# Kernel optimization log

Hardware: AMD Instinct MI355X
Metric: run time of the kernel (lower is better)

The kernel has to match this reference:

```python
import jax, jax.numpy as jnp
import numpy as np

B, T, D, H = 4, 1024, 1024, 16
DH = D // H  # 64

def setup_inputs() -> dict:
    key = jax.random.key(0)
    ks = jax.random.split(key, 5)
    s = 1.0 / np.sqrt(D)
    return {
        "x": jax.random.normal(ks[0], (B, T, D), dtype=jnp.float32),
        "Wqkv": jax.random.uniform(ks[1], (D, 3 * D), dtype=jnp.float32, minval=-s, maxval=s),
        "bqkv": jax.random.uniform(ks[2], (3 * D,), dtype=jnp.float32, minval=-s, maxval=s),
        "Wproj": jax.random.uniform(ks[3], (D, D), dtype=jnp.float32, minval=-s, maxval=s),
        "bproj": jax.random.uniform(ks[4], (D,), dtype=jnp.float32, minval=-s, maxval=s),
        "mask": jnp.ones((B, T), dtype=jnp.int32),
    }

def reference(x, Wqkv, bqkv, Wproj, bproj, mask):
    Bx, Tx, C = x.shape
    qkv = x @ Wqkv + bqkv                      # [B,T,3D]
    q, k, v = jnp.split(qkv, 3, axis=-1)
    # [B,H,T,DH]
    q = q.reshape(Bx, Tx, H, DH).transpose(0, 2, 1, 3)
    k = k.reshape(Bx, Tx, H, DH).transpose(0, 2, 1, 3)
    v = v.reshape(Bx, Tx, H, DH).transpose(0, 2, 1, 3)
    att = jnp.einsum("bhqd,bhkd->bhqk", q, k) / np.sqrt(DH)
    causal = jnp.tril(jnp.ones((Tx, Tx), dtype=bool))          # [T,T]
    keep = causal[None, None] & (mask[:, None, None, :] != 0)  # [B,1,T,T] broadcast
    att = jnp.where(keep, att, -jnp.inf)
    att = jax.nn.softmax(att, axis=-1)
    # dropout is identity in eval / p=0
    out = jnp.einsum("bhqk,bhkd->bhqd", att, v)                # [B,H,T,DH]
    out = out.transpose(0, 2, 1, 3).reshape(Bx, Tx, C)
    return out @ Wproj + bproj
```

## Files before the change

kernel.cpp:

```cpp
#include <hip/hip_runtime.h>
#include <hip/hip_bf16.h>
#include <cstddef>
#include <cstdint>

#define Bb 4
#define Tt 1024
#define Dd 1024
#define Hh 16

typedef __bf16 bf16x8 __attribute__((ext_vector_type(8)));
typedef __bf16 bf16x4 __attribute__((ext_vector_type(4)));
typedef float  f32x4  __attribute__((ext_vector_type(4)));

__device__ __forceinline__ void gload16(const void* g, void* l) {
    __builtin_amdgcn_global_load_lds(
        (const __attribute__((address_space(1))) void*)g,
        (__attribute__((address_space(3))) void*)l, 16, 0, 0);
}

__global__ __launch_bounds__(256) void prep(const float* __restrict__ x,
                                            const float* __restrict__ Wqkv,
                                            const float* __restrict__ Wproj,
                                            __bf16* __restrict__ xb,
                                            __bf16* __restrict__ wqT,
                                            __bf16* __restrict__ wpT) {
    const int bid = blockIdx.x;
    if (bid < 4096) {
        int i = bid * 256 + threadIdx.x;
        float4 v = ((const float4*)x)[i];
        bf16x4 o = { (__bf16)v.x, (__bf16)v.y, (__bf16)v.z, (__bf16)v.w };
        ((bf16x4*)xb)[i] = o;
        return;
    }
    __shared__ float ld[64][65];
    const float* in;
    __bf16* out;
    int K, N, k0, n0;
    if (bid < 4096 + 768) {
        int j = bid - 4096;
        in = Wqkv; out = wqT; K = 1024; N = 3072;
        k0 = (j & 15) * 64; n0 = (j >> 4) * 64;
    } else {
        int j = bid - 4096 - 768;
        in = Wproj; out = wpT; K = 1024; N = 1024;
        k0 = (j & 15) * 64; n0 = (j >> 4) * 64;
    }
    #pragma unroll
    for (int i = 0; i < 16; i++) {
        int idx = i * 256 + threadIdx.x;
        int r = idx >> 6, c = idx & 63;
        ld[r][c] = in[(size_t)(k0 + r) * N + n0 + c];
    }
    __syncthreads();
    #pragma unroll
    for (int i = 0; i < 16; i++) {
        int idx = i * 256 + threadIdx.x;
        int r = idx >> 6, c = idx & 63;
        out[(size_t)(n0 + r) * K + k0 + c] = (__bf16)ld[c][r];
    }
}

__global__ __launch_bounds__(256) void v_transpose(const __bf16* __restrict__ qkv,
                                                   __bf16* __restrict__ vt) {
    __shared__ __bf16 ld[64][65];
    const int t0 = blockIdx.x * 64;
    const int h  = blockIdx.y;
    const int b  = blockIdx.z;
    const size_t src = ((size_t)(b * Tt + t0)) * 3072 + 2048 + h * 64;
    #pragma unroll
    for (int i = 0; i < 16; i++) {
        int idx = i * 256 + threadIdx.x;
        int tr = idx >> 6, dc = idx & 63;
        ld[tr][dc] = qkv[src + (size_t)tr * 3072 + dc];
    }
    __syncthreads();
    const size_t dst = ((size_t)((b * Hh + h) * 64)) * Tt + t0;
    #pragma unroll
    for (int i = 0; i < 16; i++) {
        int idx = i * 256 + threadIdx.x;
        int dr = idx >> 6, tc = idx & 63;
        vt[dst + (size_t)dr * Tt + tc] = ld[tc][dr];
    }
}

__global__ __launch_bounds__(256) void gemm_bf16(const __bf16* __restrict__ A,
                                                 const __bf16* __restrict__ Bt,
                                                 const float* __restrict__ bias,
                                                 void* __restrict__ Cout,
                                                 int M, int N, int K, int mode) {
    __shared__ __align__(16) __bf16 As[128 * 64];
    __shared__ __align__(16) __bf16 Bs[128 * 64];
    const int tid  = threadIdx.x;
    const int lane = tid & 63;
    const int wave = tid >> 6;
    const int wy = wave >> 1, wx = wave & 1;
    const int l15 = lane & 15, quad = lane >> 4;
    const size_t row0 = (size_t)blockIdx.y * 128;
    const size_t col0 = (size_t)blockIdx.x * 128;

    f32x4 acc[4][4] = {};

    for (int k0 = 0; k0 < K; k0 += 64) {
        #pragma unroll
        for (int i = 0; i < 4; i++) {
            int c = i * 256 + tid;
            int r = c >> 3, seg = (c & 7) ^ (r & 7);
            gload16(&A[(row0 + r) * K + k0 + seg * 8], &As[c * 8]);
        }
        #pragma unroll
        for (int i = 0; i < 4; i++) {
            int c = i * 256 + tid;
            int r = c >> 3, seg = (c & 7) ^ (r & 7);
            gload16(&Bt[(col0 + r) * K + k0 + seg * 8], &Bs[c * 8]);
        }
        __syncthreads();
        #pragma unroll
        for (int kc = 0; kc < 2; kc++) {
            bf16x8 af[4], bfr[4];
            #pragma unroll
            for (int i = 0; i < 4; i++)
                af[i] = *(const bf16x8*)&As[(wy * 64 + i * 16 + l15) * 64 +
                                            (((kc * 4 + quad) ^ (l15 & 7)) * 8)];
            #pragma unroll
            for (int j = 0; j < 4; j++)
                bfr[j] = *(const bf16x8*)&Bs[(wx * 64 + j * 16 + l15) * 64 +
                                             (((kc * 4 + quad) ^ (l15 & 7)) * 8)];
            #pragma unroll
            for (int i = 0; i < 4; i++)
                #pragma unroll
                for (int j = 0; j < 4; j++)
                    acc[i][j] = __builtin_amdgcn_mfma_f32_16x16x32_bf16(af[i], bfr[j], acc[i][j], 0, 0, 0);
        }
        __syncthreads();
    }

    #pragma unroll
    for (int j = 0; j < 4; j++) {
        const size_t col = col0 + wx * 64 + j * 16 + l15;
        const float bj = bias[col];
        const float scale = (mode == 1 && col < 1024) ? 0.125f : 1.0f;
        #pragma unroll
        for (int i = 0; i < 4; i++) {
            const size_t row = row0 + wy * 64 + i * 16 + quad * 4;
            #pragma unroll
            for (int r = 0; r < 4; r++) {
                float v = (acc[i][j][r] + bj) * scale;
                if (mode == 1) ((__bf16*)Cout)[(row + r) * N + col] = (__bf16)v;
                else           ((float*)Cout)[(row + r) * N + col] = v;
            }
        }
    }
}

__global__ __launch_bounds__(256) void gemm_bf16_n64(const __bf16* __restrict__ A,
                                                     const __bf16* __restrict__ Bt,
                                                     const float* __restrict__ bias,
                                                     float* __restrict__ Cout,
                                                     int M, int N, int K) {
    __shared__ __align__(16) __bf16 As[128 * 64];
    __shared__ __align__(16) __bf16 Bs[64 * 64];
    const int tid  = threadIdx.x;
    const int lane = tid & 63;
    const int wave = tid >> 6;
    const int wy = wave >> 1, wx = wave & 1;
    const int l15 = lane & 15, quad = lane >> 4;
    const size_t row0 = (size_t)blockIdx.y * 128;
    const size_t col0 = (size_t)blockIdx.x * 64;

    f32x4 acc[4][2] = {};

    for (int k0 = 0; k0 < K; k0 += 64) {
        #pragma unroll
        for (int i = 0; i < 4; i++) {
            int c = i * 256 + tid;
            int r = c >> 3, seg = (c & 7) ^ (r & 7);
            gload16(&A[(row0 + r) * K + k0 + seg * 8], &As[c * 8]);
        }
        #pragma unroll
        for (int i = 0; i < 2; i++) {
            int c = i * 256 + tid;
            int r = c >> 3, seg = (c & 7) ^ (r & 7);
            gload16(&Bt[(col0 + r) * K + k0 + seg * 8], &Bs[c * 8]);
        }
        __syncthreads();
        #pragma unroll
        for (int kc = 0; kc < 2; kc++) {
            bf16x8 af[4], bfr[2];
            #pragma unroll
            for (int i = 0; i < 4; i++)
                af[i] = *(const bf16x8*)&As[(wy * 64 + i * 16 + l15) * 64 +
                                            (((kc * 4 + quad) ^ (l15 & 7)) * 8)];
            #pragma unroll
            for (int j = 0; j < 2; j++)
                bfr[j] = *(const bf16x8*)&Bs[(wx * 32 + j * 16 + l15) * 64 +
                                             (((kc * 4 + quad) ^ (l15 & 7)) * 8)];
            #pragma unroll
            for (int i = 0; i < 4; i++)
                #pragma unroll
                for (int j = 0; j < 2; j++)
                    acc[i][j] = __builtin_amdgcn_mfma_f32_16x16x32_bf16(af[i], bfr[j], acc[i][j], 0, 0, 0);
        }
        __syncthreads();
    }

    #pragma unroll
    for (int j = 0; j < 2; j++) {
        const size_t col = col0 + wx * 32 + j * 16 + l15;
        const float bj = bias[col];
        #pragma unroll
        for (int i = 0; i < 4; i++) {
            const size_t row = row0 + wy * 64 + i * 16 + quad * 4;
            #pragma unroll
            for (int r = 0; r < 4; r++)
                Cout[(row + r) * N + col] = acc[i][j][r] + bj;
        }
    }
}

__global__ __launch_bounds__(256, 3) void attn_mfma(const __bf16* __restrict__ qkv,
                                                    const __bf16* __restrict__ vt,
                                                    const int* __restrict__ mask,
                                                    __bf16* __restrict__ att) {
    __shared__ __align__(16) __bf16 smem[3 * 64 * 64];
    __bf16* const Ks = smem;
    __bf16* const Vs = smem + 4096;
    __bf16* const Ps = smem + 8192;

    const int p = blockIdx.x, h = blockIdx.y, b = blockIdx.z;
    const int qlo = p, qhi = 15 - p, nk = 16 - p;
    const int tid = threadIdx.x, lane = tid & 63, wave = tid >> 6;
    const int l15 = lane & 15, quad = lane >> 4;

    #pragma unroll
    for (int i = 0; i < 4; i++) {
        int c = i * 256 + tid;
        int rr = c >> 3, ch = c & 7;
        int w_ = rr >> 5, s_ = (rr >> 4) & 1, r16 = rr & 15;
        int grow = (s_ ? qhi : qlo) * 64 + w_ * 16 + r16;
        gload16(&qkv[((size_t)(b * Tt + grow)) * 3072 + h * 64 + ((ch ^ (rr & 7)) * 8)],
                &smem[c * 8]);
    }
    __syncthreads();
    bf16x8 qf[2][2];
    #pragma unroll
    for (int s = 0; s < 2; s++) {
        const int rowb = wave * 32 + s * 16 + l15;
        qf[s][0] = *(const bf16x8*)&smem[rowb * 64 + ((quad ^ (l15 & 7)) * 8)];
        qf[s][1] = *(const bf16x8*)&smem[rowb * 64 + (((4 + quad) ^ (l15 & 7)) * 8)];
    }
    __syncthreads();

    #pragma unroll
    for (int i = 0; i < 2; i++) {
        int c = i * 256 + tid;
        int rr = c >> 3, ch = c & 7, sw = ((ch ^ (rr & 7)) * 8);
        gload16(&qkv[((size_t)(b * Tt + rr)) * 3072 + 1024 + h * 64 + sw], &Ks[c * 8]);
        gload16(&vt[((size_t)((b * Hh + h) * 64 + rr)) * Tt + sw], &Vs[c * 8]);
    }

    f32x4 Oacc[2][4] = {};
    float lsum[2] = { 0.0f, 0.0f };

    for (int kt = 0; kt < nk; kt++) {
        __syncthreads();

        bf16x8 ak[4][2], av[4][2];
        #pragma unroll
        for (int j = 0; j < 4; j++)
            #pragma unroll
            for (int kc = 0; kc < 2; kc++) {
                int sw = (((kc * 4 + quad) ^ (l15 & 7)) * 8);
                ak[j][kc] = *(const bf16x8*)&Ks[(j * 16 + l15) * 64 + sw];
                av[j][kc] = *(const bf16x8*)&Vs[(j * 16 + l15) * 64 + sw];
            }
        __syncthreads();

        if (kt + 1 < nk) {
            #pragma unroll
            for (int i = 0; i < 2; i++) {
                int c = i * 256 + tid;
                int rr = c >> 3, ch = c & 7, sw = ((ch ^ (rr & 7)) * 8);
                gload16(&qkv[((size_t)(b * Tt + (kt + 1) * 64 + rr)) * 3072 + 1024 + h * 64 + sw],
                        &Ks[c * 8]);
                gload16(&vt[((size_t)((b * Hh + h) * 64 + rr)) * Tt + (kt + 1) * 64 + sw],
                        &Vs[c * 8]);
            }
        }

        int mv4[4][4];
        #pragma unroll
        for (int j = 0; j < 4; j++) {
            const int4 m4 = *(const int4*)&mask[b * Tt + kt * 64 + j * 16 + quad * 4];
            mv4[j][0] = m4.x; mv4[j][1] = m4.y; mv4[j][2] = m4.z; mv4[j][3] = m4.w;
        }

        #pragma unroll
        for (int s = 1; s >= 0; s--) {
            if (s == 0 && kt > qlo) continue;
            const int tile = s ? qhi : qlo;
            #pragma unroll
            for (int j = 0; j < 4; j++) {
                f32x4 st = {};
                st = __builtin_amdgcn_mfma_f32_16x16x32_bf16(ak[j][0], qf[s][0], st, 0, 0, 0);
                st = __builtin_amdgcn_mfma_f32_16x16x32_bf16(ak[j][1], qf[s][1], st, 0, 0, 0);
                bf16x4 pv;
                #pragma unroll
                for (int r = 0; r < 4; r++) {
                    const int tloc = j * 16 + quad * 4 + r;
                    bool keep = (mv4[j][r] != 0);
                    if (kt == tile) keep = keep && (tloc <= wave * 16 + l15);
                    const float pe = keep ? __expf(st[r]) : 0.0f;
                    lsum[s] += pe;
                    pv[r] = (__bf16)pe;
                }
                *(bf16x4*)&Ps[wave * 1024 + l15 * 64 + (((j * 4 + quad) ^ ((l15 & 7) << 1)) * 4)] = pv;
            }
            bf16x8 p0 = *(const bf16x8*)&Ps[wave * 1024 + l15 * 64 + (((2 * quad) ^ ((l15 & 7) << 1)) * 4)];
            bf16x8 p1 = *(const bf16x8*)&Ps[wave * 1024 + l15 * 64 + (((2 * (4 + quad)) ^ ((l15 & 7) << 1)) * 4)];
            #pragma unroll
            for (int n = 0; n < 4; n++) {
                Oacc[s][n] = __builtin_amdgcn_mfma_f32_16x16x32_bf16(av[n][0], p0, Oacc[s][n], 0, 0, 0);
                Oacc[s][n] = __builtin_amdgcn_mfma_f32_16x16x32_bf16(av[n][1], p1, Oacc[s][n], 0, 0, 0);
            }
        }
    }

    #pragma unroll
    for (int s = 0; s < 2; s++) {
        const int tile = s ? qhi : qlo;
        float lt = lsum[s];
        lt += __shfl_xor(lt, 16);
        lt += __shfl_xor(lt, 32);
        const float inv = 1.0f / lt;
        const int q = tile * 64 + wave * 16 + l15;
        #pragma unroll
        for (int n = 0; n < 4; n++) {
            bf16x4 o;
            #pragma unroll
            for (int r = 0; r < 4; r++) o[r] = (__bf16)(Oacc[s][n][r] * inv);
            *(bf16x4*)&att[((size_t)(b * Tt + q)) * Dd + h * 64 + n * 16 + quad * 4] = o;
        }
    }
}

extern "C" void kernel_launch(void* const* d_in, const int* in_sizes, int n_in,
                              void* d_out, int out_size, void* d_ws, size_t ws_size,
                              hipStream_t stream) {
    const float* x     = (const float*)d_in[0];
    const float* Wqkv  = (const float*)d_in[1];
    const float* bqkv  = (const float*)d_in[2];
    const float* Wproj = (const float*)d_in[3];
    const float* bproj = (const float*)d_in[4];
    const int*   mask  = (const int*)d_in[5];
    float* out = (float*)d_out;

    __bf16* xb  = (__bf16*)d_ws;
    __bf16* wqT = xb  + (size_t)4096 * 1024;
    __bf16* wpT = wqT + (size_t)3072 * 1024;
    __bf16* qkv = wpT + (size_t)1024 * 1024;
    __bf16* vt  = qkv + (size_t)4096 * 3072;
    __bf16* att = vt  + (size_t)4 * 16 * 64 * 1024;

    prep<<<4096 + 768 + 256, 256, 0, stream>>>(x, Wqkv, Wproj, xb, wqT, wpT);

    gemm_bf16<<<dim3(24, 32), 256, 0, stream>>>(xb, wqT, bqkv, qkv, 4096, 3072, 1024, 1);

    v_transpose<<<dim3(16, 16, 4), 256, 0, stream>>>(qkv, vt);
    attn_mfma<<<dim3(8, 16, 4), 256, 0, stream>>>(qkv, vt, mask, att);

    gemm_bf16_n64<<<dim3(16, 32), 256, 0, stream>>>(att, wpT, bproj, out, 4096, 1024, 1024);
}
```

Measured before the change: 194.1 us.

## Split attention into one block per query tile and load K/V directly from global

Each block now handles a single 64-row query tile instead of a balanced pair of tiles (qlo and qhi), which doubles the grid to 1024 blocks. K and V fragments are read straight from global memory into registers instead of being staged through double-buffered shared memory with barriers. This removes the per-iteration syncthreads and cuts LDS usage to one 64x64 buffer, which raises occupancy. In exchange the causal load balance is lost (block work now ranges from 1 to 16 K tiles), and each wave re-reads K/V from global/L2 with no LDS sharing, so memory traffic goes up.

```diff
diff --git a/kernel.cpp b/kernel.cpp
--- a/kernel.cpp
+++ b/kernel.cpp
@@ -221,72 +221,43 @@
                                                     const __bf16* __restrict__ vt,
                                                     const int* __restrict__ mask,
                                                     __bf16* __restrict__ att) {
-    __shared__ __align__(16) __bf16 smem[3 * 64 * 64];
-    __bf16* const Ks = smem;
-    __bf16* const Vs = smem + 4096;
-    __bf16* const Ps = smem + 8192;
-
-    const int p = blockIdx.x, h = blockIdx.y, b = blockIdx.z;
-    const int qlo = p, qhi = 15 - p, nk = 16 - p;
+    __shared__ __align__(16) __bf16 smem[64 * 64];
+
+    const int h  = blockIdx.x & 15;
+    const int b  = blockIdx.x >> 4;
+    const int qt = blockIdx.y;
     const int tid = threadIdx.x, lane = tid & 63, wave = tid >> 6;
     const int l15 = lane & 15, quad = lane >> 4;
 
     #pragma unroll
-    for (int i = 0; i < 4; i++) {
+    for (int i = 0; i < 2; i++) {
         int c = i * 256 + tid;
         int rr = c >> 3, ch = c & 7;
-        int w_ = rr >> 5, s_ = (rr >> 4) & 1, r16 = rr & 15;
-        int grow = (s_ ? qhi : qlo) * 64 + w_ * 16 + r16;
-        gload16(&qkv[((size_t)(b * Tt + grow)) * 3072 + h * 64 + ((ch ^ (rr & 7)) * 8)],
+        gload16(&qkv[((size_t)(b * Tt + qt * 64 + rr)) * 3072 + h * 64 + ((ch ^ (rr & 7)) * 8)],
                 &smem[c * 8]);
     }
     __syncthreads();
-    bf16x8 qf[2][2];
-    #pragma unroll
-    for (int s = 0; s < 2; s++) {
-        const int rowb = wave * 32 + s * 16 + l15;
-        qf[s][0] = *(const bf16x8*)&smem[rowb * 64 + ((quad ^ (l15 & 7)) * 8)];
-        qf[s][1] = *(const bf16x8*)&smem[rowb * 64 + (((4 + quad) ^ (l15 & 7)) * 8)];
-    }
-    __syncthreads();
-
-    #pragma unroll
-    for (int i = 0; i < 2; i++) {
-        int c = i * 256 + tid;
-        int rr = c >> 3, ch = c & 7, sw = ((ch ^ (rr & 7)) * 8);
-        gload16(&qkv[((size_t)(b * Tt + rr)) * 3072 + 1024 + h * 64 + sw], &Ks[c * 8]);
-        gload16(&vt[((size_t)((b * Hh + h) * 64 + rr)) * Tt + sw], &Vs[c * 8]);
-    }
-
-    f32x4 Oacc[2][4] = {};
-    float lsum[2] = { 0.0f, 0.0f };
-
-    for (int kt = 0; kt < nk; kt++) {
-        __syncthreads();
-
+    bf16x8 qf0 = *(const bf16x8*)&smem[(wave * 16 + l15) * 64 + ((quad ^ (l15 & 7)) * 8)];
+    bf16x8 qf1 = *(const bf16x8*)&smem[(wave * 16 + l15) * 64 + (((4 + quad) ^ (l15 & 7)) * 8)];
+    __bf16* const Ps = &smem[wave * 1024];
+
+    f32x4 Oacc[4] = {};
+    float lsum = 0.0f;
+
+    const size_t kbase = (size_t)b * Tt * 3072 + 1024 + h * 64;
+    const size_t vbase = (size_t)((b * Hh + h) * 64) * Tt;
+
+    for (int kt = 0; kt <= qt; kt++) {
         bf16x8 ak[4][2], av[4][2];
         #pragma unroll
-        for (int j = 0; j < 4; j++)
-            #pragma unroll
-            for (int kc = 0; kc < 2; kc++) {
-                int sw = (((kc * 4 + quad) ^ (l15 & 7)) * 8);
-                ak[j][kc] = *(const bf16x8*)&Ks[(j * 16 + l15) * 64 + sw];
-                av[j][kc] = *(const bf16x8*)&Vs[(j * 16 + l15) * 64 + sw];
-            }
-        __syncthreads();
-
-        if (kt + 1 < nk) {
-            #pragma unroll
-            for (int i = 0; i < 2; i++) {
-                int c = i * 256 + tid;
-                int rr = c >> 3, ch = c & 7, sw = ((ch ^ (rr & 7)) * 8);
-                gload16(&qkv[((size_t)(b * Tt + (kt + 1) * 64 + rr)) * 3072 + 1024 + h * 64 + sw],
-                        &Ks[c * 8]);
-                gload16(&vt[((size_t)((b * Hh + h) * 64 + rr)) * Tt + (kt + 1) * 64 + sw],
-                        &Vs[c * 8]);
-            }
-        }
-
+        for (int j = 0; j < 4; j++) {
+            const size_t krow = kbase + (size_t)(kt * 64 + j * 16 + l15) * 3072 + quad * 8;
+            ak[j][0] = *(const bf16x8*)&qkv[krow];
+            ak[j][1] = *(const bf16x8*)&qkv[krow + 32];
+            const size_t vrow = vbase + (size_t)(j * 16 + l15) * Tt + kt * 64 + quad * 8;
+            av[j][0] = *(const bf16x8*)&vt[vrow];
+            av[j][1] = *(const bf16x8*)&vt[vrow + 32];
+        }
         int mv4[4][4];
         #pragma unroll
         for (int j = 0; j < 4; j++) {
@@ -295,51 +266,42 @@
         }
 
         #pragma unroll
-        for (int s = 1; s >= 0; s--) {
-            if (s == 0 && kt > qlo) continue;
-            const int tile = s ? qhi : qlo;
-            #pragma unroll
-            for (int j = 0; j < 4; j++) {
-                f32x4 st = {};
-                st = __builtin_amdgcn_mfma_f32_16x16x32_bf16(ak[j][0], qf[s][0], st, 0, 0, 0);
-                st = __builtin_amdgcn_mfma_f32_16x16x32_bf16(ak[j][1], qf[s][1], st, 0, 0, 0);
-                bf16x4 pv;
-                #pragma unroll
-                for (int r = 0; r < 4; r++) {
-                    const int tloc = j * 16 + quad * 4 + r;
-                    bool keep = (mv4[j][r] != 0);
-                    if (kt == tile) keep = keep && (tloc <= wave * 16 + l15);
-                    const float pe = keep ? __expf(st[r]) : 0.0f;
-                    lsum[s] += pe;
-                    pv[r] = (__bf16)pe;
-                }
-                *(bf16x4*)&Ps[wave * 1024 + l15 * 64 + (((j * 4 + quad) ^ ((l15 & 7) << 1)) * 4)] = pv;
+        for (int j = 0; j < 4; j++) {
+            f32x4 st = {};
+            st = __builtin_amdgcn_mfma_f32_16x16x32_bf16(ak[j][0], qf0, st, 0, 0, 0);
+            st = __builtin_amdgcn_mfma_f32_16x16x32_bf16(ak[j][1], qf1, st, 0, 0, 0);
+            bf16x4 pv;
+            #pragma unroll
+            for (int r = 0; r < 4; r++) {
+                const int tloc = j * 16 + quad * 4 + r;
+                bool keep = (mv4[j][r] != 0);
+                if (kt == qt) keep = keep && (tloc <= wave * 16 + l15);
+                const float pe = keep ? __expf(st[r]) : 0.0f;
+                lsum += pe;
+                pv[r] = (__bf16)pe;
             }
-            bf16x8 p0 = *(const bf16x8*)&Ps[wave * 1024 + l15 * 64 + (((2 * quad) ^ ((l15 & 7) << 1)) * 4)];
-            bf16x8 p1 = *(const bf16x8*)&Ps[wave * 1024 + l15 * 64 + (((2 * (4 + quad)) ^ ((l15 & 7) << 1)) * 4)];
-            #pragma unroll
-            for (int n = 0; n < 4; n++) {
-                Oacc[s][n] = __builtin_amdgcn_mfma_f32_16x16x32_bf16(av[n][0], p0, Oacc[s][n], 0, 0, 0);
-                Oacc[s][n] = __builtin_amdgcn_mfma_f32_16x16x32_bf16(av[n][1], p1, Oacc[s][n], 0, 0, 0);
-            }
-        }
-    }
-
-    #pragma unroll
-    for (int s = 0; s < 2; s++) {
-        const int tile = s ? qhi : qlo;
-        float lt = lsum[s];
-        lt += __shfl_xor(lt, 16);
-        lt += __shfl_xor(lt, 32);
-        const float inv = 1.0f / lt;
-        const int q = tile * 64 + wave * 16 + l15;
+            *(bf16x4*)&Ps[l15 * 64 + (((j * 4 + quad) ^ ((l15 & 7) << 1)) * 4)] = pv;
+        }
+        bf16x8 p0 = *(const bf16x8*)&Ps[l15 * 64 + (((2 * quad) ^ ((l15 & 7) << 1)) * 4)];
+        bf16x8 p1 = *(const bf16x8*)&Ps[l15 * 64 + (((2 * (4 + quad)) ^ ((l15 & 7) << 1)) * 4)];
         #pragma unroll
         for (int n = 0; n < 4; n++) {
-            bf16x4 o;
-            #pragma unroll
-            for (int r = 0; r < 4; r++) o[r] = (__bf16)(Oacc[s][n][r] * inv);
-            *(bf16x4*)&att[((size_t)(b * Tt + q)) * Dd + h * 64 + n * 16 + quad * 4] = o;
-        }
+            Oacc[n] = __builtin_amdgcn_mfma_f32_16x16x32_bf16(av[n][0], p0, Oacc[n], 0, 0, 0);
+            Oacc[n] = __builtin_amdgcn_mfma_f32_16x16x32_bf16(av[n][1], p1, Oacc[n], 0, 0, 0);
+        }
+    }
+
+    float lt = lsum;
+    lt += __shfl_xor(lt, 16);
+    lt += __shfl_xor(lt, 32);
+    const float inv = 1.0f / lt;
+    const int q = qt * 64 + wave * 16 + l15;
+    #pragma unroll
+    for (int n = 0; n < 4; n++) {
+        bf16x4 o;
+        #pragma unroll
+        for (int r = 0; r < 4; r++) o[r] = (__bf16)(Oacc[n][r] * inv);
+        *(bf16x4*)&att[((size_t)(b * Tt + q)) * Dd + h * 64 + n * 16 + quad * 4] = o;
     }
 }
 
@@ -366,7 +328,7 @@
     gemm_bf16<<<dim3(24, 32), 256, 0, stream>>>(xb, wqT, bqkv, qkv, 4096, 3072, 1024, 1);
 
     v_transpose<<<dim3(16, 16, 4), 256, 0, stream>>>(qkv, vt);
-    attn_mfma<<<dim3(8, 16, 4), 256, 0, stream>>>(qkv, vt, mask, att);
+    attn_mfma<<<dim3(64, 16), 256, 0, stream>>>(qkv, vt, mask, att);
 
     gemm_bf16_n64<<<dim3(16, 32), 256, 0, stream>>>(att, wpT, bproj, out, 4096, 1024, 1024);
 }
```

After: 225.6 us. 1.16x slower.
